# Performance work log

Measured on AMD Instinct MI355X. Metric: run time of the kernel, lower is better.

The kernel has to match this reference:

```python
import jax, jax.numpy as jnp
import numpy as np

D_MODEL = 1024
N_HEAD = 16
D_HEAD = D_MODEL // N_HEAD


def setup_inputs() -> dict:
    key = jax.random.key(0)
    ks = jax.random.split(key, 5)
    x = jax.random.normal(ks[0], (4, 2048, D_MODEL), dtype=jnp.float32)
    s = 1.0 / np.sqrt(D_MODEL)
    W_qkv = jax.random.normal(ks[1], (D_MODEL, 3 * D_MODEL), dtype=jnp.float32) * s
    b_qkv = jnp.zeros((3 * D_MODEL,), dtype=jnp.float32)
    W_out = jax.random.normal(ks[2], (D_MODEL, D_MODEL), dtype=jnp.float32) * s
    b_out = jnp.zeros((D_MODEL,), dtype=jnp.float32)
    return {"x": x, "W_qkv": W_qkv, "b_qkv": b_qkv, "W_out": W_out, "b_out": b_out}


def reference(x, W_qkv, b_qkv, W_out, b_out):
    B, T, C = x.shape
    qkv = x @ W_qkv + b_qkv                      # [B,T,3C]
    q, k, v = jnp.split(qkv, 3, axis=-1)
    def heads(t):
        return t.reshape(B, T, N_HEAD, D_HEAD).transpose(0, 2, 1, 3)  # [B,H,T,Dh]
    q, k, v = heads(q), heads(k), heads(v)
    scale = 1.0 / np.sqrt(D_HEAD)
    attn = jnp.einsum('bhqd,bhkd->bhqk', q, k) * scale  # [B,H,T,T]
    causal = jnp.tril(jnp.ones((T, T), dtype=bool))
    attn = jnp.where(causal, attn, -jnp.inf)
    attn = jax.nn.softmax(attn, axis=-1)
    out = jnp.einsum('bhqk,bhkd->bhqd', attn, v)  # [B,H,T,Dh]
    out = out.transpose(0, 2, 1, 3).reshape(B, T, C)
    return out @ W_out + b_out
```

## Files before the change

### kernel.cpp

```cpp
#include <hip/hip_runtime.h>

typedef __bf16 bf16;
typedef __bf16 bf16x4 __attribute__((ext_vector_type(4)));
typedef __bf16 bf16x8 __attribute__((ext_vector_type(8)));
typedef float f32x4 __attribute__((ext_vector_type(4)));

#define AS1C(p) ((const __attribute__((address_space(1))) void*)(p))
#define AS3(p)  ((__attribute__((address_space(3))) void*)(p))

#define T_SEQ 2048
#define QK_LD 2048

extern "C" __device__ float __ocml_native_exp2_f32(float);

__global__ void cvt_f32_bf16(const float* __restrict__ X, bf16* __restrict__ Y, int n) {
    int i = (blockIdx.x * 256 + threadIdx.x) * 4;
    if (i >= n) return;
    const float4 f = *(const float4*)(X + i);
    bf16x4 o;
    o.x = (bf16)f.x; o.y = (bf16)f.y; o.z = (bf16)f.z; o.w = (bf16)f.w;
    *(bf16x4*)(Y + i) = o;
}

__global__ void transpose_cvt(const float* __restrict__ W, bf16* __restrict__ Wt,
                              int R, int C) {
    __shared__ float tile[32][33];
    const int bx = blockIdx.x * 32;
    const int by = blockIdx.y * 32;
    const int tx = threadIdx.x, ty = threadIdx.y;
#pragma unroll
    for (int i = 0; i < 32; i += 8)
        tile[ty + i][tx] = W[(size_t)(by + ty + i) * C + bx + tx];
    __syncthreads();
#pragma unroll
    for (int i = 0; i < 32; i += 8)
        Wt[(size_t)(bx + ty + i) * R + by + tx] = (bf16)tile[tx][ty + i];
}

template <bool OUT_BF16, bool SPLIT_V>
__global__ __launch_bounds__(256, 4)
void gemm_bt(const bf16* __restrict__ A, const bf16* __restrict__ Bt,
             const float* __restrict__ bias, void* __restrict__ Cout,
             bf16* __restrict__ Vtb, int M, int N, int K, int ldC) {
    __shared__ bf16 sm[16384];

    const int t = threadIdx.x;
    const int lane = t & 63, quad = lane >> 4, l16 = lane & 15;
    const int wave = t >> 6;
    const int wm = (wave >> 1) * 64;
    const int wn = (wave & 1) * 64;
    const long m0 = (long)blockIdx.y * 128;
    const long n0 = (long)blockIdx.x * 128;

    f32x4 acc[4][4] = {};

    const int srow = t >> 2;
    const int skb  = (t & 3) ^ ((srow >> 1) & 3);
    const bf16* aptr0 = A  + (m0 + srow) * (long)K + skb * 8;
    const bf16* aptr1 = aptr0 + (long)64 * K;
    const bf16* bptr0 = Bt + (n0 + srow) * (long)K + skb * 8;
    const bf16* bptr1 = bptr0 + (long)64 * K;

    int offA[4], offB[4];
#pragma unroll
    for (int i = 0; i < 4; ++i) {
        const int row = wm + i * 16 + l16;
        offA[i] = (row * 4 + (quad ^ ((row >> 1) & 3))) * 8;
    }
#pragma unroll
    for (int j = 0; j < 4; ++j) {
        const int row = wn + j * 16 + l16;
        offB[j] = 4096 + (row * 4 + (quad ^ ((row >> 1) & 3))) * 8;
    }

    auto stage = [&](int buf, int k0) {
        bf16* base = &sm[buf * 8192];
        __builtin_amdgcn_global_load_lds(AS1C(aptr0 + k0), AS3(base + t * 8),        16, 0, 0);
        __builtin_amdgcn_global_load_lds(AS1C(aptr1 + k0), AS3(base + 2048 + t * 8), 16, 0, 0);
        __builtin_amdgcn_global_load_lds(AS1C(bptr0 + k0), AS3(base + 4096 + t * 8), 16, 0, 0);
        __builtin_amdgcn_global_load_lds(AS1C(bptr1 + k0), AS3(base + 6144 + t * 8), 16, 0, 0);
    };
    auto compute = [&](int buf) {
        const bf16* s = &sm[buf * 8192];
        bf16x8 af[4], bfr[4];
#pragma unroll
        for (int i = 0; i < 4; ++i) af[i] = *(const bf16x8*)(s + offA[i]);
#pragma unroll
        for (int j = 0; j < 4; ++j) bfr[j] = *(const bf16x8*)(s + offB[j]);
#pragma unroll
        for (int i = 0; i < 4; ++i)
#pragma unroll
            for (int j = 0; j < 4; ++j)
                acc[i][j] = __builtin_amdgcn_mfma_f32_16x16x32_bf16(bfr[j], af[i], acc[i][j], 0, 0, 0);
    };

    stage(0, 0);
    for (int k0 = 0; k0 < K; k0 += 64) {
        __syncthreads();
        if (k0 + 32 < K) stage(1, k0 + 32);
        compute(0);
        __syncthreads();
        if (k0 + 64 < K) stage(0, k0 + 64);
        compute(1);
    }

    bf16*  Cb = (bf16*)Cout;
    float* Cf = (float*)Cout;
    const bool vblock = SPLIT_V && (n0 >= 2048);
#pragma unroll
    for (int i = 0; i < 4; ++i) {
        const long gm = m0 + wm + i * 16 + l16;
#pragma unroll
        for (int j = 0; j < 4; ++j) {
            const int nloc = wn + j * 16 + quad * 4;
            const long n = n0 + nloc;
            const float4 bv = *(const float4*)(bias + n);
            float v[4];
#pragma unroll
            for (int r = 0; r < 4; ++r) v[r] = acc[i][j][r] + (&bv.x)[r];
            if (vblock) {
                const int bb = (int)(gm >> 11), tok = (int)(gm & 2047);
                const int nv = (int)(n - 2048);
                const int h = nv >> 6, d0 = nv & 63;
                bf16* dst = Vtb + ((size_t)(bb * 16 + h) * 64 + d0) * T_SEQ + tok;
#pragma unroll
                for (int r = 0; r < 4; ++r) dst[(size_t)r * T_SEQ] = (bf16)v[r];
            } else if (OUT_BF16) {
                bf16x4 o;
#pragma unroll
                for (int r = 0; r < 4; ++r) o[r] = (bf16)v[r];
                *(bf16x4*)(Cb + gm * ldC + n) = o;
            } else {
                float4 o;
#pragma unroll
                for (int r = 0; r < 4; ++r) (&o.x)[r] = v[r];
                *(float4*)(Cf + gm * ldC + n) = o;
            }
        }
    }
}

__global__ __launch_bounds__(256, 3)
void attn_kernel(const bf16* __restrict__ qk, const bf16* __restrict__ vtb,
                 bf16* __restrict__ Out) {
    const int bh = blockIdx.x;
    const int qt = 15 - (int)blockIdx.y;
    const int b = bh >> 4, h = bh & 15;
    const int t = threadIdx.x;
    const int wave = t >> 6, lane = t & 63, quad = lane >> 4, l16 = lane & 15;
    const int wq = wave * 32;
    const int q0 = qt * 128;

    __shared__ bf16 Ks[2][4096];
    __shared__ bf16 VTs[2][4096];
    __shared__ bf16 Ps[8192];

    const bf16* Qg = qk + (size_t)b * T_SEQ * QK_LD + h * 64;
    const bf16* Kg = Qg + 1024;
    const bf16* vth = vtb + (size_t)bh * 64 * T_SEQ;

    for (int c = t; c < 1024; c += 256) {
        const int row = c >> 3, kb = c & 7;
        *(uint4*)(Ps + row * 64 + (((kb ^ (row & 7)) << 3))) =
            *(const uint4*)(Qg + (size_t)(q0 + row) * QK_LD + kb * 8);
    }
    __syncthreads();
    const float qsc = 0.125f * 1.4426950408889634f;
    bf16x8 qf[2][2];
#pragma unroll
    for (int jt = 0; jt < 2; ++jt)
#pragma unroll
        for (int s = 0; s < 2; ++s) {
            const int row = wq + jt * 16 + l16;
            bf16x8 v = *(const bf16x8*)(Ps + row * 64 + (((s * 4 + quad) ^ (row & 7)) << 3));
#pragma unroll
            for (int e = 0; e < 8; ++e) v[e] = (bf16)((float)v[e] * qsc);
            qf[jt][s] = v;
        }

    const int sr = t >> 3;
    const int skb = (t & 7) ^ (sr & 7);
    const bf16* kp0 = Kg + (size_t)sr * QK_LD + skb * 8;
    const bf16* kp1 = kp0 + (size_t)32 * QK_LD;
    const bf16* vp0 = vth + (size_t)sr * T_SEQ + skb * 8;
    const bf16* vp1 = vp0 + (size_t)32 * T_SEQ;

    int offKV[4][2];
#pragma unroll
    for (int it = 0; it < 4; ++it)
#pragma unroll
        for (int s = 0; s < 2; ++s) {
            const int row = it * 16 + l16;
            offKV[it][s] = row * 64 + (((s * 4 + quad) ^ (row & 7)) << 3);
        }

    f32x4 oacc[4][2] = {};
    float lsum[2] = {0.f, 0.f};
    const int nkt = qt * 2 + 2;

    uint4 kr0 = *(const uint4*)kp0, kr1 = *(const uint4*)kp1;
    uint4 vr0 = *(const uint4*)vp0, vr1 = *(const uint4*)vp1;

    for (int kt = 0; kt < nkt; ++kt) {
        const int k0 = kt * 64;
        bf16* kb_ = Ks[kt & 1];
        bf16* vb_ = VTs[kt & 1];
        *(uint4*)(kb_ + t * 8)        = kr0;
        *(uint4*)(kb_ + 2048 + t * 8) = kr1;
        *(uint4*)(vb_ + t * 8)        = vr0;
        *(uint4*)(vb_ + 2048 + t * 8) = vr1;
        __syncthreads();

        if (kt + 1 < nkt) {
            const int kn = k0 + 64;
            kr0 = *(const uint4*)(kp0 + (size_t)kn * QK_LD);
            kr1 = *(const uint4*)(kp1 + (size_t)kn * QK_LD);
            vr0 = *(const uint4*)(vp0 + kn);
            vr1 = *(const uint4*)(vp1 + kn);
        }

        f32x4 sacc[4][2] = {};
#pragma unroll
        for (int s = 0; s < 2; ++s) {
            bf16x8 kf[4];
#pragma unroll
            for (int it = 0; it < 4; ++it)
                kf[it] = *(const bf16x8*)(kb_ + offKV[it][s]);
#pragma unroll
            for (int it = 0; it < 4; ++it)
#pragma unroll
                for (int jt = 0; jt < 2; ++jt)
                    sacc[it][jt] = __builtin_amdgcn_mfma_f32_16x16x32_bf16(kf[it], qf[jt][s], sacc[it][jt], 0, 0, 0);
        }

        const bool need_mask = (kt >= 2 * qt);
#pragma unroll
        for (int it = 0; it < 4; ++it)
#pragma unroll
            for (int jt = 0; jt < 2; ++jt) {
                const int prow = wq + jt * 16 + l16;
                bf16x4 pb;
                if (need_mask) {
                    const int qrow = q0 + prow;
                    const int kbase = k0 + it * 16 + quad * 4;
#pragma unroll
                    for (int r = 0; r < 4; ++r) {
                        const float e = __ocml_native_exp2_f32(sacc[it][jt][r]);
                        const float p = (kbase + r > qrow) ? 0.f : e;
                        lsum[jt] += p;
                        pb[r] = (bf16)p;
                    }
                } else {
#pragma unroll
                    for (int r = 0; r < 4; ++r) {
                        const float p = __ocml_native_exp2_f32(sacc[it][jt][r]);
                        lsum[jt] += p;
                        pb[r] = (bf16)p;
                    }
                }
                *(bf16x4*)(Ps + prow * 64 +
                           (((it * 2 + (quad >> 1)) ^ (prow & 7)) << 3) + ((quad & 1) << 2)) = pb;
            }

#pragma unroll
        for (int s2 = 0; s2 < 2; ++s2) {
            bf16x8 vf[4], pf[2];
#pragma unroll
            for (int it2 = 0; it2 < 4; ++it2)
                vf[it2] = *(const bf16x8*)(vb_ + offKV[it2][s2]);
#pragma unroll
            for (int jt = 0; jt < 2; ++jt) {
                const int prow = wq + jt * 16 + l16;
                pf[jt] = *(const bf16x8*)(Ps + prow * 64 + (((s2 * 4 + quad) ^ (prow & 7)) << 3));
            }
#pragma unroll
            for (int it2 = 0; it2 < 4; ++it2)
#pragma unroll
                for (int jt = 0; jt < 2; ++jt)
                    oacc[it2][jt] = __builtin_amdgcn_mfma_f32_16x16x32_bf16(vf[it2], pf[jt], oacc[it2][jt], 0, 0, 0);
        }
    }

    float inv[2];
#pragma unroll
    for (int jt = 0; jt < 2; ++jt) {
        float l = lsum[jt];
        l += __shfl_xor(l, 16);
        l += __shfl_xor(l, 32);
        inv[jt] = 1.0f / l;
    }
#pragma unroll
    for (int it2 = 0; it2 < 4; ++it2)
#pragma unroll
        for (int jt = 0; jt < 2; ++jt) {
            bf16x4 ob;
#pragma unroll
            for (int r = 0; r < 4; ++r) ob[r] = (bf16)(oacc[it2][jt][r] * inv[jt]);
            const int qrow = q0 + wq + jt * 16 + l16;
            const int dcol = h * 64 + it2 * 16 + quad * 4;
            *(bf16x4*)&Out[(size_t)(b * T_SEQ + qrow) * 1024 + dcol] = ob;
        }
}

extern "C" void kernel_launch(void* const* d_in, const int* in_sizes, int n_in,
                              void* d_out, int out_size, void* d_ws, size_t ws_size,
                              hipStream_t stream) {
    const float* x     = (const float*)d_in[0];
    const float* W_qkv = (const float*)d_in[1];
    const float* b_qkv = (const float*)d_in[2];
    const float* W_out = (const float*)d_in[3];
    const float* b_out = (const float*)d_in[4];
    float* out = (float*)d_out;

    char* ws = (char*)d_ws;
    bf16* xb   = (bf16*)ws; ws += (size_t)8192 * 1024 * 2;
    bf16* wtq  = (bf16*)ws; ws += (size_t)3072 * 1024 * 2;
    bf16* wto  = (bf16*)ws; ws += (size_t)1024 * 1024 * 2;
    bf16* qkb  = (bf16*)ws; ws += (size_t)8192 * 2048 * 2;
    bf16* vtb  = (bf16*)ws; ws += (size_t)64 * 64 * 2048 * 2;
    bf16* aout = (bf16*)ws; ws += (size_t)8192 * 1024 * 2;

    cvt_f32_bf16<<<8192, 256, 0, stream>>>(x, xb, 8192 * 1024);
    transpose_cvt<<<dim3(96, 32), dim3(32, 8), 0, stream>>>(W_qkv, wtq, 1024, 3072);
    transpose_cvt<<<dim3(32, 32), dim3(32, 8), 0, stream>>>(W_out, wto, 1024, 1024);

    gemm_bt<true, true><<<dim3(24, 64), 256, 0, stream>>>(
        xb, wtq, b_qkv, (void*)qkb, vtb, 8192, 3072, 1024, 2048);
    attn_kernel<<<dim3(64, 16), 256, 0, stream>>>(qkb, vtb, aout);
    gemm_bt<false, false><<<dim3(8, 64), 256, 0, stream>>>(
        aout, wto, b_out, (void*)out, nullptr, 8192, 1024, 1024, 1024);
}
```

Before: 246.1 us.

## Replace direct global-to-LDS loads with register-staged prefetch pipeline in GEMM

The GEMM mainloop no longer uses global_load_lds to copy tiles straight into shared memory. Tiles are now loaded into registers two k-steps ahead and written to swizzled LDS before each compute step, with one barrier per step instead of two. The aim is to hide global load latency behind the MFMA work. It costs extra VGPRs for the staged tiles and explicit LDS write instructions, which may reduce occupancy under the launch bound of 4.

```diff
diff --git a/kernel.cpp b/kernel.cpp
--- a/kernel.cpp
+++ b/kernel.cpp
@@ -4,9 +4,6 @@
 typedef __bf16 bf16x4 __attribute__((ext_vector_type(4)));
 typedef __bf16 bf16x8 __attribute__((ext_vector_type(8)));
 typedef float f32x4 __attribute__((ext_vector_type(4)));
-
-#define AS1C(p) ((const __attribute__((address_space(1))) void*)(p))
-#define AS3(p)  ((__attribute__((address_space(3))) void*)(p))
 
 #define T_SEQ 2048
 #define QK_LD 2048
@@ -54,12 +51,12 @@
 
     f32x4 acc[4][4] = {};
 
-    const int srow = t >> 2;
-    const int skb  = (t & 3) ^ ((srow >> 1) & 3);
-    const bf16* aptr0 = A  + (m0 + srow) * (long)K + skb * 8;
-    const bf16* aptr1 = aptr0 + (long)64 * K;
-    const bf16* bptr0 = Bt + (n0 + srow) * (long)K + skb * 8;
-    const bf16* bptr1 = bptr0 + (long)64 * K;
+    const int sr = t >> 2, sc = t & 3;
+    const int swz  = (sr * 4 + (sc ^ ((sr >> 1) & 3))) * 8;
+    const int swz2 = ((sr + 64) * 4 + (sc ^ ((sr >> 1) & 3))) * 8;
+    const bf16* agp = A  + (m0 + sr) * (long)K + sc * 8;
+    const bf16* bgp = Bt + (n0 + sr) * (long)K + sc * 8;
+    const long rowK = (long)64 * K;
 
     int offA[4], offB[4];
 #pragma unroll
@@ -73,12 +70,20 @@
         offB[j] = 4096 + (row * 4 + (quad ^ ((row >> 1) & 3))) * 8;
     }
 
-    auto stage = [&](int buf, int k0) {
+    uint4 Ra0[2], Ra1[2], Rb0[2], Rb1[2];
+
+    auto load_set = [&](int s, int k) {
+        Ra0[s] = *(const uint4*)(agp + k);
+        Ra1[s] = *(const uint4*)(agp + rowK + k);
+        Rb0[s] = *(const uint4*)(bgp + k);
+        Rb1[s] = *(const uint4*)(bgp + rowK + k);
+    };
+    auto write_set = [&](int s, int buf) {
         bf16* base = &sm[buf * 8192];
-        __builtin_amdgcn_global_load_lds(AS1C(aptr0 + k0), AS3(base + t * 8),        16, 0, 0);
-        __builtin_amdgcn_global_load_lds(AS1C(aptr1 + k0), AS3(base + 2048 + t * 8), 16, 0, 0);
-        __builtin_amdgcn_global_load_lds(AS1C(bptr0 + k0), AS3(base + 4096 + t * 8), 16, 0, 0);
-        __builtin_amdgcn_global_load_lds(AS1C(bptr1 + k0), AS3(base + 6144 + t * 8), 16, 0, 0);
+        *(uint4*)(base + swz)         = Ra0[s];
+        *(uint4*)(base + swz2)        = Ra1[s];
+        *(uint4*)(base + 4096 + swz)  = Rb0[s];
+        *(uint4*)(base + 4096 + swz2) = Rb1[s];
     };
     auto compute = [&](int buf) {
         const bf16* s = &sm[buf * 8192];
@@ -94,14 +99,20 @@
                 acc[i][j] = __builtin_amdgcn_mfma_f32_16x16x32_bf16(bfr[j], af[i], acc[i][j], 0, 0, 0);
     };
 
-    stage(0, 0);
-    for (int k0 = 0; k0 < K; k0 += 64) {
-        __syncthreads();
-        if (k0 + 32 < K) stage(1, k0 + 32);
-        compute(0);
-        __syncthreads();
-        if (k0 + 64 < K) stage(0, k0 + 64);
-        compute(1);
+    const int nk = K >> 5;
+    load_set(0, 0);
+    load_set(1, 32);
+    write_set(0, 0);
+    load_set(0, 64);
+    __syncthreads();
+
+    for (int kk = 0; kk < nk; ++kk) {
+        if (kk + 1 < nk) {
+            write_set((kk + 1) & 1, (kk + 1) & 1);
+            if (kk + 3 < nk) load_set((kk + 1) & 1, (kk + 3) * 32);
+        }
+        compute(kk & 1);
+        if (kk + 1 < nk) __syncthreads();
     }
 
     bf16*  Cb = (bf16*)Cout;
```

Result: slower. 488.8 us (+98.6%).

## Enlarge GEMM and attention tiles to 256 rows per block

Applied to the files above, without the earlier changes.

The GEMM block tile grows from 128x128 to 256x128. Each wave now owns 64 rows across all 128 columns, so B fragments are reused across more MFMAs and fewer blocks are launched. The attention kernel moves to 256-query tiles with 64 rows per wave, and waves skip key tiles that lie entirely above their causal diagonal. The change roughly doubles accumulator registers and LDS per block and lowers occupancy hints to 2. It also halves the grid size, which risks under-filling the GPU's CUs and creating load imbalance in causal attention.

```diff
diff --git a/kernel.cpp b/kernel.cpp
--- a/kernel.cpp
+++ b/kernel.cpp
@@ -38,69 +38,72 @@
 }
 
 template <bool OUT_BF16, bool SPLIT_V>
-__global__ __launch_bounds__(256, 4)
+__global__ __launch_bounds__(256, 2)
 void gemm_bt(const bf16* __restrict__ A, const bf16* __restrict__ Bt,
              const float* __restrict__ bias, void* __restrict__ Cout,
              bf16* __restrict__ Vtb, int M, int N, int K, int ldC) {
-    __shared__ bf16 sm[16384];
+    __shared__ bf16 sm[24576];
 
     const int t = threadIdx.x;
     const int lane = t & 63, quad = lane >> 4, l16 = lane & 15;
     const int wave = t >> 6;
-    const int wm = (wave >> 1) * 64;
-    const int wn = (wave & 1) * 64;
-    const long m0 = (long)blockIdx.y * 128;
+    const int wm = wave * 64;
+    const long m0 = (long)blockIdx.y * 256;
     const long n0 = (long)blockIdx.x * 128;
 
-    f32x4 acc[4][4] = {};
-
-    const int srow = t >> 2;
-    const int skb  = (t & 3) ^ ((srow >> 1) & 3);
-    const bf16* aptr0 = A  + (m0 + srow) * (long)K + skb * 8;
-    const bf16* aptr1 = aptr0 + (long)64 * K;
-    const bf16* bptr0 = Bt + (n0 + srow) * (long)K + skb * 8;
-    const bf16* bptr1 = bptr0 + (long)64 * K;
-
-    int offA[4], offB[4];
+    f32x4 acc[4][8] = {};
+
+    const int sr = t >> 2, sc = t & 3;
+    const int skb = sc ^ ((sr >> 1) & 3);
+    const bf16* agp = A  + (m0 + sr) * (long)K + skb * 8;
+    const bf16* bgp = Bt + (n0 + sr) * (long)K + skb * 8;
+    const long rowK = (long)64 * K;
+
+    int offA[4], offB[8];
 #pragma unroll
     for (int i = 0; i < 4; ++i) {
         const int row = wm + i * 16 + l16;
         offA[i] = (row * 4 + (quad ^ ((row >> 1) & 3))) * 8;
     }
 #pragma unroll
-    for (int j = 0; j < 4; ++j) {
-        const int row = wn + j * 16 + l16;
-        offB[j] = 4096 + (row * 4 + (quad ^ ((row >> 1) & 3))) * 8;
+    for (int j = 0; j < 8; ++j) {
+        const int row = j * 16 + l16;
+        offB[j] = 8192 + (row * 4 + (quad ^ ((row >> 1) & 3))) * 8;
     }
 
     auto stage = [&](int buf, int k0) {
-        bf16* base = &sm[buf * 8192];
-        __builtin_amdgcn_global_load_lds(AS1C(aptr0 + k0), AS3(base + t * 8),        16, 0, 0);
-        __builtin_amdgcn_global_load_lds(AS1C(aptr1 + k0), AS3(base + 2048 + t * 8), 16, 0, 0);
-        __builtin_amdgcn_global_load_lds(AS1C(bptr0 + k0), AS3(base + 4096 + t * 8), 16, 0, 0);
-        __builtin_amdgcn_global_load_lds(AS1C(bptr1 + k0), AS3(base + 6144 + t * 8), 16, 0, 0);
+        bf16* base = &sm[buf * 12288];
+#pragma unroll
+        for (int i = 0; i < 4; ++i)
+            __builtin_amdgcn_global_load_lds(AS1C(agp + i * rowK + k0),
+                                             AS3(base + i * 2048 + t * 8), 16, 0, 0);
+#pragma unroll
+        for (int i = 0; i < 2; ++i)
+            __builtin_amdgcn_global_load_lds(AS1C(bgp + i * rowK + k0),
+                                             AS3(base + 8192 + i * 2048 + t * 8), 16, 0, 0);
     };
     auto compute = [&](int buf) {
-        const bf16* s = &sm[buf * 8192];
-        bf16x8 af[4], bfr[4];
+        const bf16* s = &sm[buf * 12288];
+        bf16x8 af[4], bfr[8];
 #pragma unroll
         for (int i = 0; i < 4; ++i) af[i] = *(const bf16x8*)(s + offA[i]);
 #pragma unroll
-        for (int j = 0; j < 4; ++j) bfr[j] = *(const bf16x8*)(s + offB[j]);
+        for (int j = 0; j < 8; ++j) bfr[j] = *(const bf16x8*)(s + offB[j]);
 #pragma unroll
         for (int i = 0; i < 4; ++i)
 #pragma unroll
-            for (int j = 0; j < 4; ++j)
+            for (int j = 0; j < 8; ++j)
                 acc[i][j] = __builtin_amdgcn_mfma_f32_16x16x32_bf16(bfr[j], af[i], acc[i][j], 0, 0, 0);
     };
 
+    const int nk = K >> 5;
     stage(0, 0);
-    for (int k0 = 0; k0 < K; k0 += 64) {
+    for (int kk = 0; kk < nk; kk += 2) {
         __syncthreads();
-        if (k0 + 32 < K) stage(1, k0 + 32);
+        if (kk + 1 < nk) stage(1, (kk + 1) * 32);
         compute(0);
         __syncthreads();
-        if (k0 + 64 < K) stage(0, k0 + 64);
+        if (kk + 2 < nk) stage(0, (kk + 2) * 32);
         compute(1);
     }
 
@@ -111,9 +114,8 @@
     for (int i = 0; i < 4; ++i) {
         const long gm = m0 + wm + i * 16 + l16;
 #pragma unroll
-        for (int j = 0; j < 4; ++j) {
-            const int nloc = wn + j * 16 + quad * 4;
-            const long n = n0 + nloc;
+        for (int j = 0; j < 8; ++j) {
+            const long n = n0 + j * 16 + quad * 4;
             const float4 bv = *(const float4*)(bias + n);
             float v[4];
 #pragma unroll
@@ -140,35 +142,35 @@
     }
 }
 
-__global__ __launch_bounds__(256, 3)
+__global__ __launch_bounds__(256, 2)
 void attn_kernel(const bf16* __restrict__ qk, const bf16* __restrict__ vtb,
                  bf16* __restrict__ Out) {
     const int bh = blockIdx.x;
-    const int qt = 15 - (int)blockIdx.y;
+    const int qt = 7 - (int)blockIdx.y;
     const int b = bh >> 4, h = bh & 15;
     const int t = threadIdx.x;
     const int wave = t >> 6, lane = t & 63, quad = lane >> 4, l16 = lane & 15;
-    const int wq = wave * 32;
-    const int q0 = qt * 128;
+    const int wq = wave * 64;
+    const int q0 = qt * 256;
 
     __shared__ bf16 Ks[2][4096];
     __shared__ bf16 VTs[2][4096];
-    __shared__ bf16 Ps[8192];
+    __shared__ bf16 Ps[16384];
 
     const bf16* Qg = qk + (size_t)b * T_SEQ * QK_LD + h * 64;
     const bf16* Kg = Qg + 1024;
     const bf16* vth = vtb + (size_t)bh * 64 * T_SEQ;
 
-    for (int c = t; c < 1024; c += 256) {
+    for (int c = t; c < 2048; c += 256) {
         const int row = c >> 3, kb = c & 7;
-        *(uint4*)(Ps + row * 64 + (((kb ^ (row & 7)) << 3))) =
+        *(uint4*)(Ps + row * 64 + ((kb ^ (row & 7)) << 3)) =
             *(const uint4*)(Qg + (size_t)(q0 + row) * QK_LD + kb * 8);
     }
     __syncthreads();
     const float qsc = 0.125f * 1.4426950408889634f;
-    bf16x8 qf[2][2];
-#pragma unroll
-    for (int jt = 0; jt < 2; ++jt)
+    bf16x8 qf[4][2];
+#pragma unroll
+    for (int jt = 0; jt < 4; ++jt)
 #pragma unroll
         for (int s = 0; s < 2; ++s) {
             const int row = wq + jt * 16 + l16;
@@ -194,9 +196,9 @@
             offKV[it][s] = row * 64 + (((s * 4 + quad) ^ (row & 7)) << 3);
         }
 
-    f32x4 oacc[4][2] = {};
-    float lsum[2] = {0.f, 0.f};
-    const int nkt = qt * 2 + 2;
+    f32x4 oacc[4][4] = {};
+    float lsum[4] = {0.f, 0.f, 0.f, 0.f};
+    const int nkt = (qt + 1) * 4;
 
     uint4 kr0 = *(const uint4*)kp0, kr1 = *(const uint4*)kp1;
     uint4 vr0 = *(const uint4*)vp0, vr1 = *(const uint4*)vp1;
@@ -219,7 +221,9 @@
             vr1 = *(const uint4*)(vp1 + kn);
         }
 
-        f32x4 sacc[4][2] = {};
+        if (k0 > q0 + wq + 63) continue;
+
+        f32x4 sacc[4][4] = {};
 #pragma unroll
         for (int s = 0; s < 2; ++s) {
             bf16x8 kf[4];
@@ -229,15 +233,15 @@
 #pragma unroll
             for (int it = 0; it < 4; ++it)
 #pragma unroll
-                for (int jt = 0; jt < 2; ++jt)
+                for (int jt = 0; jt < 4; ++jt)
                     sacc[it][jt] = __builtin_amdgcn_mfma_f32_16x16x32_bf16(kf[it], qf[jt][s], sacc[it][jt], 0, 0, 0);
         }
 
-        const bool need_mask = (kt >= 2 * qt);
+        const bool need_mask = (k0 + 63 > q0 + wq);
 #pragma unroll
         for (int it = 0; it < 4; ++it)
 #pragma unroll
-            for (int jt = 0; jt < 2; ++jt) {
+            for (int jt = 0; jt < 4; ++jt) {
                 const int prow = wq + jt * 16 + l16;
                 bf16x4 pb;
                 if (need_mask) {
@@ -264,26 +268,26 @@
 
 #pragma unroll
         for (int s2 = 0; s2 < 2; ++s2) {
-            bf16x8 vf[4], pf[2];
+            bf16x8 vf[4], pf[4];
 #pragma unroll
             for (int it2 = 0; it2 < 4; ++it2)
                 vf[it2] = *(const bf16x8*)(vb_ + offKV[it2][s2]);
 #pragma unroll
-            for (int jt = 0; jt < 2; ++jt) {
+            for (int jt = 0; jt < 4; ++jt) {
                 const int prow = wq + jt * 16 + l16;
                 pf[jt] = *(const bf16x8*)(Ps + prow * 64 + (((s2 * 4 + quad) ^ (prow & 7)) << 3));
             }
 #pragma unroll
             for (int it2 = 0; it2 < 4; ++it2)
 #pragma unroll
-                for (int jt = 0; jt < 2; ++jt)
+                for (int jt = 0; jt < 4; ++jt)
                     oacc[it2][jt] = __builtin_amdgcn_mfma_f32_16x16x32_bf16(vf[it2], pf[jt], oacc[it2][jt], 0, 0, 0);
         }
     }
 
-    float inv[2];
-#pragma unroll
-    for (int jt = 0; jt < 2; ++jt) {
+    float inv[4];
+#pragma unroll
+    for (int jt = 0; jt < 4; ++jt) {
         float l = lsum[jt];
         l += __shfl_xor(l, 16);
         l += __shfl_xor(l, 32);
@@ -292,7 +296,7 @@
 #pragma unroll
     for (int it2 = 0; it2 < 4; ++it2)
 #pragma unroll
-        for (int jt = 0; jt < 2; ++jt) {
+        for (int jt = 0; jt < 4; ++jt) {
             bf16x4 ob;
 #pragma unroll
             for (int r = 0; r < 4; ++r) ob[r] = (bf16)(oacc[it2][jt][r] * inv[jt]);
@@ -324,9 +328,9 @@
     transpose_cvt<<<dim3(96, 32), dim3(32, 8), 0, stream>>>(W_qkv, wtq, 1024, 3072);
     transpose_cvt<<<dim3(32, 32), dim3(32, 8), 0, stream>>>(W_out, wto, 1024, 1024);
 
-    gemm_bt<true, true><<<dim3(24, 64), 256, 0, stream>>>(
+    gemm_bt<true, true><<<dim3(24, 32), 256, 0, stream>>>(
         xb, wtq, b_qkv, (void*)qkb, vtb, 8192, 3072, 1024, 2048);
-    attn_kernel<<<dim3(64, 16), 256, 0, stream>>>(qkb, vtb, aout);
-    gemm_bt<false, false><<<dim3(8, 64), 256, 0, stream>>>(
+    attn_kernel<<<dim3(64, 8), 256, 0, stream>>>(qkb, vtb, aout);
+    gemm_bt<false, false><<<dim3(8, 32), 256, 0, stream>>>(
         aout, wto, b_out, (void*)out, nullptr, 8192, 1024, 1024, 1024);
 }
```

Result: slower. 270.9 us (+10.1%).

## Load GEMM A-fragments and attention K/V fragments directly from global into registers

Applied to the files above, without the earlier changes.

In the GEMM, only the B tile is staged through LDS. Each wave now loads its A fragments straight from global memory into registers, one step ahead, which halves LDS traffic and LDS size and lowers the launch bound to 3. In attention, K and V MFMA fragments are loaded directly from global memory into registers and prefetched one tile ahead, which drops the K/V shared buffers and the per-tile barrier. The cost is more register pressure and uncoalesced global loads that are duplicated across waves, since each wave refetches the full K/V tile.

```diff
diff --git a/kernel.cpp b/kernel.cpp
--- a/kernel.cpp
+++ b/kernel.cpp
@@ -38,11 +38,11 @@
 }
 
 template <bool OUT_BF16, bool SPLIT_V>
-__global__ __launch_bounds__(256, 4)
+__global__ __launch_bounds__(256, 3)
 void gemm_bt(const bf16* __restrict__ A, const bf16* __restrict__ Bt,
              const float* __restrict__ bias, void* __restrict__ Cout,
              bf16* __restrict__ Vtb, int M, int N, int K, int ldC) {
-    __shared__ bf16 sm[16384];
+    __shared__ bf16 Bs[2][4096];
 
     const int t = threadIdx.x;
     const int lane = t & 63, quad = lane >> 4, l16 = lane & 15;
@@ -54,54 +54,69 @@
 
     f32x4 acc[4][4] = {};
 
-    const int srow = t >> 2;
-    const int skb  = (t & 3) ^ ((srow >> 1) & 3);
-    const bf16* aptr0 = A  + (m0 + srow) * (long)K + skb * 8;
-    const bf16* aptr1 = aptr0 + (long)64 * K;
-    const bf16* bptr0 = Bt + (n0 + srow) * (long)K + skb * 8;
-    const bf16* bptr1 = bptr0 + (long)64 * K;
-
-    int offA[4], offB[4];
-#pragma unroll
-    for (int i = 0; i < 4; ++i) {
-        const int row = wm + i * 16 + l16;
-        offA[i] = (row * 4 + (quad ^ ((row >> 1) & 3))) * 8;
-    }
+    const int sr = t >> 2, sc = t & 3;
+    const int skb = sc ^ ((sr >> 1) & 3);
+    const bf16* bgp = Bt + (n0 + sr) * (long)K + skb * 8;
+    const long rowK64 = (long)64 * K;
+
+    int offB[4];
 #pragma unroll
     for (int j = 0; j < 4; ++j) {
         const int row = wn + j * 16 + l16;
-        offB[j] = 4096 + (row * 4 + (quad ^ ((row >> 1) & 3))) * 8;
-    }
-
-    auto stage = [&](int buf, int k0) {
-        bf16* base = &sm[buf * 8192];
-        __builtin_amdgcn_global_load_lds(AS1C(aptr0 + k0), AS3(base + t * 8),        16, 0, 0);
-        __builtin_amdgcn_global_load_lds(AS1C(aptr1 + k0), AS3(base + 2048 + t * 8), 16, 0, 0);
-        __builtin_amdgcn_global_load_lds(AS1C(bptr0 + k0), AS3(base + 4096 + t * 8), 16, 0, 0);
-        __builtin_amdgcn_global_load_lds(AS1C(bptr1 + k0), AS3(base + 6144 + t * 8), 16, 0, 0);
+        offB[j] = (row * 4 + (quad ^ ((row >> 1) & 3))) * 8;
+    }
+
+    const bf16* ap = A + (m0 + wm + l16) * (long)K + quad * 8;
+    const long aK16 = (long)16 * K;
+
+    auto stageB = [&](int buf, int k0) {
+        __builtin_amdgcn_global_load_lds(AS1C(bgp + k0),          AS3(&Bs[buf][0] + t * 8), 16, 0, 0);
+        __builtin_amdgcn_global_load_lds(AS1C(bgp + rowK64 + k0), AS3(&Bs[buf][2048] + t * 8), 16, 0, 0);
     };
-    auto compute = [&](int buf) {
-        const bf16* s = &sm[buf * 8192];
-        bf16x8 af[4], bfr[4];
-#pragma unroll
-        for (int i = 0; i < 4; ++i) af[i] = *(const bf16x8*)(s + offA[i]);
-#pragma unroll
-        for (int j = 0; j < 4; ++j) bfr[j] = *(const bf16x8*)(s + offB[j]);
+
+    bf16x8 afA[4], afB[4];
+
+    const int nk = K >> 5;
+    stageB(0, 0);
+#pragma unroll
+    for (int i = 0; i < 4; ++i) afA[i] = *(const bf16x8*)(ap + i * aK16);
+    __syncthreads();
+
+    for (int kk = 0; kk < nk; kk += 2) {
+        stageB(1, (kk + 1) * 32);
 #pragma unroll
         for (int i = 0; i < 4; ++i)
-#pragma unroll
-            for (int j = 0; j < 4; ++j)
-                acc[i][j] = __builtin_amdgcn_mfma_f32_16x16x32_bf16(bfr[j], af[i], acc[i][j], 0, 0, 0);
-    };
-
-    stage(0, 0);
-    for (int k0 = 0; k0 < K; k0 += 64) {
+            afB[i] = *(const bf16x8*)(ap + i * aK16 + (kk + 1) * 32L);
+        {
+            const bf16* s = &Bs[0][0];
+            bf16x8 bfr[4];
+#pragma unroll
+            for (int j = 0; j < 4; ++j) bfr[j] = *(const bf16x8*)(s + offB[j]);
+#pragma unroll
+            for (int i = 0; i < 4; ++i)
+#pragma unroll
+                for (int j = 0; j < 4; ++j)
+                    acc[i][j] = __builtin_amdgcn_mfma_f32_16x16x32_bf16(bfr[j], afA[i], acc[i][j], 0, 0, 0);
+        }
         __syncthreads();
-        if (k0 + 32 < K) stage(1, k0 + 32);
-        compute(0);
-        __syncthreads();
-        if (k0 + 64 < K) stage(0, k0 + 64);
-        compute(1);
+        if (kk + 2 < nk) {
+            stageB(0, (kk + 2) * 32);
+#pragma unroll
+            for (int i = 0; i < 4; ++i)
+                afA[i] = *(const bf16x8*)(ap + i * aK16 + (kk + 2) * 32L);
+        }
+        {
+            const bf16* s = &Bs[1][0];
+            bf16x8 bfr[4];
+#pragma unroll
+            for (int j = 0; j < 4; ++j) bfr[j] = *(const bf16x8*)(s + offB[j]);
+#pragma unroll
+            for (int i = 0; i < 4; ++i)
+#pragma unroll
+                for (int j = 0; j < 4; ++j)
+                    acc[i][j] = __builtin_amdgcn_mfma_f32_16x16x32_bf16(bfr[j], afB[i], acc[i][j], 0, 0, 0);
+        }
+        if (kk + 2 < nk) __syncthreads();
     }
 
     bf16*  Cb = (bf16*)Cout;
@@ -121,8 +136,8 @@
             if (vblock) {
                 const int bb = (int)(gm >> 11), tok = (int)(gm & 2047);
                 const int nv = (int)(n - 2048);
-                const int h = nv >> 6, d0 = nv & 63;
-                bf16* dst = Vtb + ((size_t)(bb * 16 + h) * 64 + d0) * T_SEQ + tok;
+                const int hh = nv >> 6, d0 = nv & 63;
+                bf16* dst = Vtb + ((size_t)(bb * 16 + hh) * 64 + d0) * T_SEQ + tok;
 #pragma unroll
                 for (int r = 0; r < 4; ++r) dst[(size_t)r * T_SEQ] = (bf16)v[r];
             } else if (OUT_BF16) {
@@ -151,8 +166,6 @@
     const int wq = wave * 32;
     const int q0 = qt * 128;
 
-    __shared__ bf16 Ks[2][4096];
-    __shared__ bf16 VTs[2][4096];
     __shared__ bf16 Ps[8192];
 
     const bf16* Qg = qk + (size_t)b * T_SEQ * QK_LD + h * 64;
@@ -161,7 +174,7 @@
 
     for (int c = t; c < 1024; c += 256) {
         const int row = c >> 3, kb = c & 7;
-        *(uint4*)(Ps + row * 64 + (((kb ^ (row & 7)) << 3))) =
+        *(uint4*)(Ps + row * 64 + ((kb ^ (row & 7)) << 3)) =
             *(const uint4*)(Qg + (size_t)(q0 + row) * QK_LD + kb * 8);
     }
     __syncthreads();
@@ -178,59 +191,53 @@
             qf[jt][s] = v;
         }
 
-    const int sr = t >> 3;
-    const int skb = (t & 7) ^ (sr & 7);
-    const bf16* kp0 = Kg + (size_t)sr * QK_LD + skb * 8;
-    const bf16* kp1 = kp0 + (size_t)32 * QK_LD;
-    const bf16* vp0 = vth + (size_t)sr * T_SEQ + skb * 8;
-    const bf16* vp1 = vp0 + (size_t)32 * T_SEQ;
-
-    int offKV[4][2];
+    int pwOff[2][4], pfOff[2][2];
+#pragma unroll
+    for (int jt = 0; jt < 2; ++jt) {
+        const int prow = wq + jt * 16 + l16;
+#pragma unroll
+        for (int it = 0; it < 4; ++it)
+            pwOff[jt][it] = prow * 64 + (((it * 2 + (quad >> 1)) ^ (prow & 7)) << 3) + ((quad & 1) << 2);
+#pragma unroll
+        for (int s2 = 0; s2 < 2; ++s2)
+            pfOff[jt][s2] = prow * 64 + (((s2 * 4 + quad) ^ (prow & 7)) << 3);
+    }
+
+    const bf16* kfp = Kg + (size_t)l16 * QK_LD + quad * 8;
+    const bf16* vfp = vth + (size_t)l16 * T_SEQ + quad * 8;
+
+    bf16x8 kf[4][2], vf[4][2];
 #pragma unroll
     for (int it = 0; it < 4; ++it)
 #pragma unroll
         for (int s = 0; s < 2; ++s) {
-            const int row = it * 16 + l16;
-            offKV[it][s] = row * 64 + (((s * 4 + quad) ^ (row & 7)) << 3);
+            kf[it][s] = *(const bf16x8*)(kfp + (size_t)it * 16 * QK_LD + s * 32);
+            vf[it][s] = *(const bf16x8*)(vfp + (size_t)it * 16 * T_SEQ + s * 32);
         }
 
     f32x4 oacc[4][2] = {};
     float lsum[2] = {0.f, 0.f};
     const int nkt = qt * 2 + 2;
 
-    uint4 kr0 = *(const uint4*)kp0, kr1 = *(const uint4*)kp1;
-    uint4 vr0 = *(const uint4*)vp0, vr1 = *(const uint4*)vp1;
-
     for (int kt = 0; kt < nkt; ++kt) {
         const int k0 = kt * 64;
-        bf16* kb_ = Ks[kt & 1];
-        bf16* vb_ = VTs[kt & 1];
-        *(uint4*)(kb_ + t * 8)        = kr0;
-        *(uint4*)(kb_ + 2048 + t * 8) = kr1;
-        *(uint4*)(vb_ + t * 8)        = vr0;
-        *(uint4*)(vb_ + 2048 + t * 8) = vr1;
-        __syncthreads();
+
+        f32x4 sacc[4][2] = {};
+#pragma unroll
+        for (int s = 0; s < 2; ++s)
+#pragma unroll
+            for (int it = 0; it < 4; ++it)
+#pragma unroll
+                for (int jt = 0; jt < 2; ++jt)
+                    sacc[it][jt] = __builtin_amdgcn_mfma_f32_16x16x32_bf16(kf[it][s], qf[jt][s], sacc[it][jt], 0, 0, 0);
 
         if (kt + 1 < nkt) {
-            const int kn = k0 + 64;
-            kr0 = *(const uint4*)(kp0 + (size_t)kn * QK_LD);
-            kr1 = *(const uint4*)(kp1 + (size_t)kn * QK_LD);
-            vr0 = *(const uint4*)(vp0 + kn);
-            vr1 = *(const uint4*)(vp1 + kn);
-        }
-
-        f32x4 sacc[4][2] = {};
-#pragma unroll
-        for (int s = 0; s < 2; ++s) {
-            bf16x8 kf[4];
+            const bf16* kn = kfp + (size_t)(k0 + 64) * QK_LD;
 #pragma unroll
             for (int it = 0; it < 4; ++it)
-                kf[it] = *(const bf16x8*)(kb_ + offKV[it][s]);
-#pragma unroll
-            for (int it = 0; it < 4; ++it)
-#pragma unroll
-                for (int jt = 0; jt < 2; ++jt)
-                    sacc[it][jt] = __builtin_amdgcn_mfma_f32_16x16x32_bf16(kf[it], qf[jt][s], sacc[it][jt], 0, 0, 0);
+#pragma unroll
+                for (int s = 0; s < 2; ++s)
+                    kf[it][s] = *(const bf16x8*)(kn + (size_t)it * 16 * QK_LD + s * 32);
         }
 
         const bool need_mask = (kt >= 2 * qt);
@@ -238,10 +245,9 @@
         for (int it = 0; it < 4; ++it)
 #pragma unroll
             for (int jt = 0; jt < 2; ++jt) {
-                const int prow = wq + jt * 16 + l16;
                 bf16x4 pb;
                 if (need_mask) {
-                    const int qrow = q0 + prow;
+                    const int qrow = q0 + wq + jt * 16 + l16;
                     const int kbase = k0 + it * 16 + quad * 4;
 #pragma unroll
                     for (int r = 0; r < 4; ++r) {
@@ -258,26 +264,29 @@
                         pb[r] = (bf16)p;
                     }
                 }
-                *(bf16x4*)(Ps + prow * 64 +
-                           (((it * 2 + (quad >> 1)) ^ (prow & 7)) << 3) + ((quad & 1) << 2)) = pb;
+                *(bf16x4*)(Ps + pwOff[jt][it]) = pb;
             }
 
 #pragma unroll
         for (int s2 = 0; s2 < 2; ++s2) {
-            bf16x8 vf[4], pf[2];
+            bf16x8 pf[2];
+#pragma unroll
+            for (int jt = 0; jt < 2; ++jt)
+                pf[jt] = *(const bf16x8*)(Ps + pfOff[jt][s2]);
 #pragma unroll
             for (int it2 = 0; it2 < 4; ++it2)
-                vf[it2] = *(const bf16x8*)(vb_ + offKV[it2][s2]);
-#pragma unroll
-            for (int jt = 0; jt < 2; ++jt) {
-                const int prow = wq + jt * 16 + l16;
-                pf[jt] = *(const bf16x8*)(Ps + prow * 64 + (((s2 * 4 + quad) ^ (prow & 7)) << 3));
-            }
-#pragma unroll
-            for (int it2 = 0; it2 < 4; ++it2)
 #pragma unroll
                 for (int jt = 0; jt < 2; ++jt)
-                    oacc[it2][jt] = __builtin_amdgcn_mfma_f32_16x16x32_bf16(vf[it2], pf[jt], oacc[it2][jt], 0, 0, 0);
+                    oacc[it2][jt] = __builtin_amdgcn_mfma_f32_16x16x32_bf16(vf[it2][s2], pf[jt], oacc[it2][jt], 0, 0, 0);
+        }
+
+        if (kt + 1 < nkt) {
+            const bf16* vn = vfp + (size_t)(k0 + 64);
+#pragma unroll
+            for (int it = 0; it < 4; ++it)
+#pragma unroll
+                for (int s = 0; s < 2; ++s)
+                    vf[it][s] = *(const bf16x8*)(vn + (size_t)it * 16 * T_SEQ + s * 32);
         }
     }
 
```

After: 428.1 us. 73.9% more time.
